# Performance work log

Measured on AMD Instinct MI355X. Metric: run time of the kernel, lower is better.

## Reference

```python
import jax, jax.numpy as jnp
import numpy as np

DIM = 512
NUM_HEADS = 8
WS = 7
HEAD_DIM = DIM // NUM_HEADS
SCALE = HEAD_DIM ** -0.5
THETA = 10000.0


def _freqs_cis_2d(hd, end):
    # 2D axial RoPE: interleaved (x,y) complex rotations per frequency
    Hg = int(end ** 0.5)
    pos = jnp.arange(end)
    x_pos = (pos % Hg).astype(jnp.float32)
    y_pos = (pos // Hg).astype(jnp.float32)
    freqs = 1.0 / THETA ** (jnp.arange(0, hd, 4)[: hd // 4].astype(jnp.float32) / hd)
    x_cis = jnp.exp(1j * jnp.outer(x_pos, freqs))  # (end, hd//4) complex64
    y_cis = jnp.exp(1j * jnp.outer(y_pos, freqs))
    return jnp.stack([x_cis, y_cis], axis=-1).reshape(end, -1)  # (end, hd//2)


def setup_inputs() -> dict:
    key = jax.random.key(0)
    k1, k2, k3 = jax.random.split(key, 3)
    B, H, W, C = 32, 56, 56, DIM
    x = jax.random.normal(k1, (B, H * W, C), dtype=jnp.float32)
    w_qkv = jax.random.normal(k2, (3 * C, C), dtype=jnp.float32) * 0.02
    w_proj = jax.random.normal(k3, (C, C), dtype=jnp.float32) * 0.02
    b_proj = jnp.zeros((C,), dtype=jnp.float32)
    return {"x": x, "w_qkv": w_qkv, "w_proj": w_proj, "b_proj": b_proj, "H": H, "W": W}


def reference(x, w_qkv, w_proj, b_proj, H, W):
    B, N, C = x.shape
    nh, hd, ws = NUM_HEADS, HEAD_DIM, WS
    _h, _w = H // ws, W // ws
    G, S = _h * _w, ws * ws
    # window partition: (B, _h, _w, ws, ws, C)
    xw = x.reshape(B, _h, ws, _w, ws, C).transpose(0, 1, 3, 2, 4, 5)
    qkv = jnp.einsum('bhwpqc,dc->bhwpqd', xw, w_qkv).reshape(B, G, S, 3, nh, hd)
    q, k, v = qkv[..., 0, :, :], qkv[..., 1, :, :], qkv[..., 2, :, :]  # (B,G,S,nh,hd)

    fc = _freqs_cis_2d(hd, S)  # (S, hd//2) complex64

    def rope(t):
        tc = t.reshape(*t.shape[:-1], hd // 2, 2)
        tc = jax.lax.complex(tc[..., 0], tc[..., 1])       # (B,G,S,nh,hd//2)
        tc = tc * fc[None, None, :, None, :]
        return jnp.stack([tc.real, tc.imag], axis=-1).reshape(t.shape)

    q = rope(q)
    k = rope(k)
    attn = jnp.einsum('bgsnd,bgtnd->bgnst', q, k) * SCALE  # (B,G,nh,S,S)
    attn = jax.nn.softmax(attn, axis=-1)
    out = jnp.einsum('bgnst,bgtnd->bgsnd', attn, v)        # (B,G,S,nh,hd)
    # window merge back to (B, H, W, C)
    out = out.reshape(B, _h, _w, ws, ws, C).transpose(0, 1, 3, 2, 4, 5).reshape(B, N, C)
    return jnp.einsum('bnc,dc->bnd', out, w_proj) + b_proj
```

## Files before the change

### kernel.cpp

```cpp
#include <hip/hip_runtime.h>
#include <stdint.h>
#include <stddef.h>

typedef _Float16 f16;
typedef _Float16 f16x8 __attribute__((ext_vector_type(8)));
typedef _Float16 f16x4 __attribute__((ext_vector_type(4)));
typedef float    f32x4 __attribute__((ext_vector_type(4)));

#define AS1 __attribute__((address_space(1)))
#define AS3 __attribute__((address_space(3)))

__device__ __forceinline__ void gl_lds16(const f16* g, f16* l) {
  __builtin_amdgcn_global_load_lds((const AS1 uint32_t*)g, (AS3 uint32_t*)l, 16, 0, 0);
}


__global__ __launch_bounds__(256) void k_prep(
    const float* __restrict__ x, const float* __restrict__ wqkv,
    const float* __restrict__ wproj,
    f16* __restrict__ x16, f16* __restrict__ wqkv16, f16* __restrict__ wproj16,
    float2* __restrict__ tab)
{
  const int XB = 25088, WQ = 384, WP = 128;
  int b = blockIdx.x, t = threadIdx.x;
  const float* src; f16* dst; long i0;
  if (b < XB)            { src = x;     dst = x16;     i0 = ((long)b*256 + t)*8; }
  else if (b < XB+WQ)    { src = wqkv;  dst = wqkv16;  i0 = ((long)(b-XB)*256 + t)*8; }
  else if (b < XB+WQ+WP) { src = wproj; dst = wproj16; i0 = ((long)(b-XB-WQ)*256 + t)*8; }
  else {
    int id = (b - XB - WQ - WP)*256 + t;
    if (id < 49*32) {
      int s = id >> 5, i = id & 31, j = i >> 1;
      float freq = expf(-(float)(4*j)*(1.0f/64.0f)*9.210340372f);
      float pos = (i & 1) ? (float)(s/7) : (float)(s%7);
      float a = pos * freq;
      tab[id] = make_float2(cosf(a), sinf(a));
    }
    return;
  }
  const float4* s4 = (const float4*)(src + i0);
  float4 v0 = s4[0], v1 = s4[1];
  f16x8 h = { (f16)v0.x,(f16)v0.y,(f16)v0.z,(f16)v0.w,
              (f16)v1.x,(f16)v1.y,(f16)v1.z,(f16)v1.w };
  *(f16x8*)(dst + i0) = h;
}

#define GEMM_STAGE(gW, gX, Wt, Xt, kt)                                        \
  {                                                                           \
    int srow = ln >> 3;                        \
    int schunk = (ln & 7) ^ srow;              \
    size_t goff = (size_t)srow * 512 + (kt)*64 + schunk * 8;                  \
    _Pragma("unroll")                                                         \
    for (int ii = 0; ii < 4; ++ii) {                                          \
      int r0 = wave * 32 + ii * 8;                                            \
      gl_lds16(gW + (size_t)r0 * 512 + goff, Wt + r0 * 64);                   \
      gl_lds16(gX + (size_t)r0 * 512 + goff, Xt + r0 * 64);                   \
    }                                                                         \
  }

#define GEMM_MAIN(Wt, Xt)                                                     \
  _Pragma("unroll")                                                           \
  for (int k2 = 0; k2 < 2; ++k2) {                                            \
    f16x8 af[4], bf[4];                                                       \
    int pc = ((k2 * 4 + quad) ^ (l15 & 7)) * 8;                               \
    _Pragma("unroll")                                                         \
    for (int i = 0; i < 4; ++i)                                               \
      af[i] = *(const f16x8*)&Wt[(wq * 64 + i * 16 + l15) * 64 + pc];         \
    _Pragma("unroll")                                                         \
    for (int j = 0; j < 4; ++j)                                               \
      bf[j] = *(const f16x8*)&Xt[(wp * 64 + j * 16 + l15) * 64 + pc];         \
    _Pragma("unroll")                                                         \
    for (int i = 0; i < 4; ++i)                                               \
      _Pragma("unroll")                                                       \
      for (int j = 0; j < 4; ++j)                                             \
        acc[i][j] = __builtin_amdgcn_mfma_f32_16x16x32_f16(af[i], bf[j],      \
                                                           acc[i][j], 0, 0, 0);\
  }

__global__ __launch_bounds__(256) void k_qkv(
    const f16* __restrict__ x16, const f16* __restrict__ w16,
    const float2* __restrict__ tab,
    f16* __restrict__ qb, f16* __restrict__ kb, f16* __restrict__ vb)
{
  __shared__ __align__(16) f16 Wt[128*64];
  __shared__ __align__(16) f16 Xt[128*64];
  const int by = blockIdx.x;
  const int bx = blockIdx.y;
  const int tid = threadIdx.x;
  const int wave = tid >> 6, ln = tid & 63;
  const int l15 = ln & 15, quad = ln >> 4;
  const int wq = wave >> 1, wp = wave & 1;

  f32x4 acc[4][4] = {};
  const f16* gW = w16 + (size_t)(by*128)*512;
  const f16* gX = x16 + (size_t)(bx*128)*512;

  for (int kt = 0; kt < 8; ++kt) {
    __syncthreads();
    GEMM_STAGE(gW, gX, Wt, Xt, kt);
    __syncthreads();
    GEMM_MAIN(Wt, Xt);
  }

  const int t = (by*128) >> 9;
#pragma unroll
  for (int j = 0; j < 4; ++j) {
    int m  = bx*128 + wp*64 + j*16 + l15;
    int b  = m / 3136;
    int nn = m - b*3136;
    int hh = nn / 56, ww = nn - hh*56;
    int gh = hh / 7,  p  = hh - gh*7;
    int gw = ww / 7,  qx = ww - gw*7;
    int g  = gh*8 + gw;
    int s  = p*7 + qx;
    int bg = b*64 + g;
#pragma unroll
    for (int i = 0; i < 4; ++i) {
      int c0   = by*128 + wq*64 + i*16 + quad*4;
      int cin  = c0 & 511;
      int head = cin >> 6;
      int dd   = cin & 63;
      float v0 = acc[i][j][0], v1 = acc[i][j][1], v2 = acc[i][j][2], v3 = acc[i][j][3];
      f16x4 h4;
      if (t < 2) {
        float2 t0 = tab[s*32 + (dd >> 1)];
        float2 t1 = tab[s*32 + (dd >> 1) + 1];
        h4[0] = (f16)(v0*t0.x - v1*t0.y);
        h4[1] = (f16)(v0*t0.y + v1*t0.x);
        h4[2] = (f16)(v2*t1.x - v3*t1.y);
        h4[3] = (f16)(v2*t1.y + v3*t1.x);
      } else {
        h4[0] = (f16)v0; h4[1] = (f16)v1; h4[2] = (f16)v2; h4[3] = (f16)v3;
      }
      f16* dst = (t == 0 ? qb : (t == 1 ? kb : vb))
               + (size_t)((bg*8 + head)*49 + s)*64 + dd;
      *(f16x4*)dst = h4;
    }
  }
}

__global__ __launch_bounds__(64) void k_attn(
    const f16* __restrict__ qb, const f16* __restrict__ kb,
    const f16* __restrict__ vb, f16* __restrict__ ob)
{
  __shared__ __align__(16) f16 Vt[64*64];
  __shared__ __align__(16) f16 P[64*72];
  __shared__ float lsum[64];
  const int bid = blockIdx.x;
  const int ln = threadIdx.x, l15 = ln & 15, quad = ln >> 4;
  const f16* q = qb + (size_t)bid*(49*64);
  const f16* k = kb + (size_t)bid*(49*64);
  const f16* v = vb + (size_t)bid*(49*64);

#pragma unroll
  for (int i = 0; i < 8; ++i)
    gl_lds16(v + (size_t)(i*8 + (ln>>3))*64 + (ln&7)*8, Vt + i*512);

  f32x4 a[4][4] = {};
#pragma unroll
  for (int kt = 0; kt < 2; ++kt) {
    f16x8 qf[4], kf[4];
#pragma unroll
    for (int mt = 0; mt < 4; ++mt) {
      int s = mt*16 + l15; if (s > 48) s = 48;
      qf[mt] = *(const f16x8*)(q + s*64 + kt*32 + quad*8);
      kf[mt] = *(const f16x8*)(k + s*64 + kt*32 + quad*8);
    }
#pragma unroll
    for (int mt = 0; mt < 4; ++mt)
#pragma unroll
      for (int nt = 0; nt < 4; ++nt)
        a[mt][nt] = __builtin_amdgcn_mfma_f32_16x16x32_f16(qf[mt], kf[nt], a[mt][nt], 0, 0, 0);
  }

  const float scale = 0.125f;
#pragma unroll
  for (int mt = 0; mt < 4; ++mt) {
    float mx[4] = {-1e30f,-1e30f,-1e30f,-1e30f};
#pragma unroll
    for (int nt = 0; nt < 4; ++nt) {
      int col = nt*16 + l15;
      bool valid = col < 49;
#pragma unroll
      for (int r = 0; r < 4; ++r) {
        float vv = valid ? a[mt][nt][r]*scale : -1e30f;
        a[mt][nt][r] = vv;
        mx[r] = fmaxf(mx[r], vv);
      }
    }
#pragma unroll
    for (int d = 1; d < 16; d <<= 1)
#pragma unroll
      for (int r = 0; r < 4; ++r) mx[r] = fmaxf(mx[r], __shfl_xor(mx[r], d, 64));
    float sm[4] = {0.f,0.f,0.f,0.f};
#pragma unroll
    for (int nt = 0; nt < 4; ++nt)
#pragma unroll
      for (int r = 0; r < 4; ++r) {
        float e = __expf(a[mt][nt][r] - mx[r]);
        a[mt][nt][r] = e;
        sm[r] += e;
      }
#pragma unroll
    for (int d = 1; d < 16; d <<= 1)
#pragma unroll
      for (int r = 0; r < 4; ++r) sm[r] += __shfl_xor(sm[r], d, 64);
#pragma unroll
    for (int nt = 0; nt < 4; ++nt)
#pragma unroll
      for (int r = 0; r < 4; ++r)
        P[(mt*16 + quad*4 + r)*72 + nt*16 + l15] = (f16)a[mt][nt][r];
    if (l15 == 0) {
#pragma unroll
      for (int r = 0; r < 4; ++r) lsum[mt*16 + quad*4 + r] = sm[r];
    }
  }
  __syncthreads();

  f32x4 o[4][4] = {};
#pragma unroll
  for (int kt = 0; kt < 2; ++kt) {
    const int s0 = kt*32 + quad*8;
    f16x8 vf[4], pf[4];
#pragma unroll
    for (int dt = 0; dt < 4; ++dt)
#pragma unroll
      for (int j = 0; j < 8; ++j)
        vf[dt][j] = Vt[(s0 + j)*64 + dt*16 + l15];
#pragma unroll
    for (int st = 0; st < 4; ++st) pf[st] = *(const f16x8*)&P[(st*16 + l15)*72 + s0];
#pragma unroll
    for (int dt = 0; dt < 4; ++dt)
#pragma unroll
      for (int st = 0; st < 4; ++st)
        o[dt][st] = __builtin_amdgcn_mfma_f32_16x16x32_f16(vf[dt], pf[st], o[dt][st], 0, 0, 0);
  }

  const int bg = bid >> 3, head = bid & 7;
#pragma unroll
  for (int st = 0; st < 4; ++st) {
    int sq = st*16 + l15;
    if (sq < 49) {
      float inv = 1.0f / lsum[sq];
#pragma unroll
      for (int dt = 0; dt < 4; ++dt) {
        int d0 = dt*16 + quad*4;
        f16x4 h4 = { (f16)(o[dt][st][0]*inv), (f16)(o[dt][st][1]*inv),
                     (f16)(o[dt][st][2]*inv), (f16)(o[dt][st][3]*inv) };
        *(f16x4*)(ob + (size_t)(bg*49 + sq)*512 + head*64 + d0) = h4;
      }
    }
  }
}

__global__ __launch_bounds__(256) void k_proj(
    const f16* __restrict__ a16, const f16* __restrict__ w16,
    const float* __restrict__ bias, float* __restrict__ out)
{
  __shared__ __align__(16) f16 Wt[128*64];
  __shared__ __align__(16) f16 Xt[128*64];
  const int by = blockIdx.x;
  const int bx = blockIdx.y;
  const int tid = threadIdx.x;
  const int wave = tid >> 6, ln = tid & 63;
  const int l15 = ln & 15, quad = ln >> 4;
  const int wq = wave >> 1, wp = wave & 1;

  f32x4 acc[4][4] = {};
  const f16* gW = w16 + (size_t)(by*128)*512;
  const f16* gX = a16 + (size_t)(bx*128)*512;

  for (int kt = 0; kt < 8; ++kt) {
    __syncthreads();
    GEMM_STAGE(gW, gX, Wt, Xt, kt);
    __syncthreads();
    GEMM_MAIN(Wt, Xt);
  }

#pragma unroll
  for (int j = 0; j < 4; ++j) {
    int m  = bx*128 + wp*64 + j*16 + l15;
    int b  = m / 3136;
    int rr = m - b*3136;
    int g  = rr / 49;
    int s  = rr - g*49;
    int gh = g >> 3, gw = g & 7;
    int p  = s / 7,  qx = s - p*7;
    int hh = gh*7 + p, ww = gw*7 + qx;
    size_t tok = (size_t)b*3136 + hh*56 + ww;
#pragma unroll
    for (int i = 0; i < 4; ++i) {
      int d0 = by*128 + wq*64 + i*16 + quad*4;
      float4 bb = *(const float4*)(bias + d0);
      float4 o4 = make_float4(acc[i][j][0]+bb.x, acc[i][j][1]+bb.y,
                              acc[i][j][2]+bb.z, acc[i][j][3]+bb.w);
      *(float4*)(out + tok*512 + d0) = o4;
    }
  }
}

extern "C" void kernel_launch(void* const* d_in, const int* in_sizes, int n_in,
                              void* d_out, int out_size, void* d_ws, size_t ws_size,
                              hipStream_t stream) {
  const float* x     = (const float*)d_in[0];
  const float* wqkv  = (const float*)d_in[1];
  const float* wproj = (const float*)d_in[2];
  const float* bias  = (const float*)d_in[3];

  char* ws = (char*)d_ws;
  f16*    x16   = (f16*)(ws);
  f16*    wq16  = (f16*)(ws + 102760448);
  f16*    wp16  = (f16*)(ws + 104333312);
  float2* tab   = (float2*)(ws + 104857600);
  f16*    vbuf  = (f16*)(ws + 104873984);
  f16*    attn16 = (f16*)(ws);

  f16* qbuf = (f16*)d_out;
  f16* kbuf = (f16*)((char*)d_out + 102760448);
  float* out = (float*)d_out;

  k_prep<<<dim3(25088 + 384 + 128 + 7), dim3(256), 0, stream>>>(
      x, wqkv, wproj, x16, wq16, wp16, tab);
  k_qkv<<<dim3(12, 784), dim3(256), 0, stream>>>(x16, wq16, tab, qbuf, kbuf, vbuf);
  k_attn<<<dim3(16384), dim3(64), 0, stream>>>(qbuf, kbuf, vbuf, attn16);
  k_proj<<<dim3(4, 784), dim3(256), 0, stream>>>(attn16, wp16, bias, out);
}
```

Before: 882.4 us.

## Double-buffer GEMM LDS tiles and remap block IDs for XCD-local reuse

The QKV and projection GEMMs now use two LDS buffers, prefetching the next K-tile with global_load_lds while MFMAs run on the current one. This removes one barrier per iteration and lets load latency overlap with compute. The grids become 1D, and block IDs are remapped so that blocks sharing the same X row tile land on the same XCD, which should improve L2 reuse. LDS use doubles to 64KB per block, which may lower occupancy, and per-lane global pointers are precomputed.

```diff
diff --git a/kernel.cpp b/kernel.cpp
--- a/kernel.cpp
+++ b/kernel.cpp
@@ -45,30 +45,37 @@
   *(f16x8*)(dst + i0) = h;
 }
 
-#define GEMM_STAGE(gW, gX, Wt, Xt, kt)                                        \
-  {                                                                           \
-    int srow = ln >> 3;                        \
-    int schunk = (ln & 7) ^ srow;              \
-    size_t goff = (size_t)srow * 512 + (kt)*64 + schunk * 8;                  \
-    _Pragma("unroll")                                                         \
-    for (int ii = 0; ii < 4; ++ii) {                                          \
-      int r0 = wave * 32 + ii * 8;                                            \
-      gl_lds16(gW + (size_t)r0 * 512 + goff, Wt + r0 * 64);                   \
-      gl_lds16(gX + (size_t)r0 * 512 + goff, Xt + r0 * 64);                   \
-    }                                                                         \
-  }
-
-#define GEMM_MAIN(Wt, Xt)                                                     \
+#define GEMM_PRELUDE()                                                        \
+  const int tid = threadIdx.x;                                                \
+  const int wave = tid >> 6, ln = tid & 63;                                   \
+  const int l15 = ln & 15, quad = ln >> 4;                                    \
+  const int wq = wave >> 1, wp = wave & 1;                                    \
+  const int srow = ln >> 3, schunk = (ln & 7) ^ srow;                         \
+  const f16* pW[4]; const f16* pX[4];                                         \
+  _Pragma("unroll")                                                           \
+  for (int ii = 0; ii < 4; ++ii) {                                            \
+    size_t ro = (size_t)(wave*32 + ii*8 + srow)*512 + schunk*8;               \
+    pW[ii] = gW + ro; pX[ii] = gX + ro;                                       \
+  }
+
+#define GEMM_STAGE(bsel, kt)                                                  \
+  _Pragma("unroll")                                                           \
+  for (int ii = 0; ii < 4; ++ii) {                                            \
+    gl_lds16(pW[ii] + (kt)*64, &Wt[bsel][(wave*32 + ii*8)*64]);               \
+    gl_lds16(pX[ii] + (kt)*64, &Xt[bsel][(wave*32 + ii*8)*64]);               \
+  }
+
+#define GEMM_MAIN(bsel)                                                       \
   _Pragma("unroll")                                                           \
   for (int k2 = 0; k2 < 2; ++k2) {                                            \
     f16x8 af[4], bf[4];                                                       \
     int pc = ((k2 * 4 + quad) ^ (l15 & 7)) * 8;                               \
     _Pragma("unroll")                                                         \
     for (int i = 0; i < 4; ++i)                                               \
-      af[i] = *(const f16x8*)&Wt[(wq * 64 + i * 16 + l15) * 64 + pc];         \
+      af[i] = *(const f16x8*)&Wt[bsel][(wq * 64 + i * 16 + l15) * 64 + pc];   \
     _Pragma("unroll")                                                         \
     for (int j = 0; j < 4; ++j)                                               \
-      bf[j] = *(const f16x8*)&Xt[(wp * 64 + j * 16 + l15) * 64 + pc];         \
+      bf[j] = *(const f16x8*)&Xt[bsel][(wp * 64 + j * 16 + l15) * 64 + pc];   \
     _Pragma("unroll")                                                         \
     for (int i = 0; i < 4; ++i)                                               \
       _Pragma("unroll")                                                       \
@@ -77,30 +84,36 @@
                                                            acc[i][j], 0, 0, 0);\
   }
 
+#define GEMM_LOOP()                                                           \
+  GEMM_STAGE(0, 0);                                                           \
+  __syncthreads();                                                            \
+  _Pragma("unroll")                                                           \
+  for (int kt = 0; kt < 8; ++kt) {                                            \
+    if (kt < 7) GEMM_STAGE((kt + 1) & 1, kt + 1);                             \
+    GEMM_MAIN(kt & 1);                                                        \
+    if (kt < 7) __syncthreads();                                              \
+  }
+
 __global__ __launch_bounds__(256) void k_qkv(
     const f16* __restrict__ x16, const f16* __restrict__ w16,
     const float2* __restrict__ tab,
     f16* __restrict__ qb, f16* __restrict__ kb, f16* __restrict__ vb)
 {
-  __shared__ __align__(16) f16 Wt[128*64];
-  __shared__ __align__(16) f16 Xt[128*64];
-  const int by = blockIdx.x;
-  const int bx = blockIdx.y;
-  const int tid = threadIdx.x;
-  const int wave = tid >> 6, ln = tid & 63;
-  const int l15 = ln & 15, quad = ln >> 4;
-  const int wq = wave >> 1, wp = wave & 1;
-
-  f32x4 acc[4][4] = {};
+  __shared__ __align__(16) f16 Wt[2][128*64];
+  __shared__ __align__(16) f16 Xt[2][128*64];
+  const int bid = blockIdx.x;
+  const int xcd = bid & 7;
+  const int jj  = bid >> 3;
+  const int qq  = jj / 12;
+  const int by  = jj - qq*12;
+  const int bx  = xcd + qq*8;
+
   const f16* gW = w16 + (size_t)(by*128)*512;
   const f16* gX = x16 + (size_t)(bx*128)*512;
-
-  for (int kt = 0; kt < 8; ++kt) {
-    __syncthreads();
-    GEMM_STAGE(gW, gX, Wt, Xt, kt);
-    __syncthreads();
-    GEMM_MAIN(Wt, Xt);
-  }
+  GEMM_PRELUDE();
+
+  f32x4 acc[4][4] = {};
+  GEMM_LOOP();
 
   const int t = (by*128) >> 9;
 #pragma unroll
@@ -257,25 +270,21 @@
     const f16* __restrict__ a16, const f16* __restrict__ w16,
     const float* __restrict__ bias, float* __restrict__ out)
 {
-  __shared__ __align__(16) f16 Wt[128*64];
-  __shared__ __align__(16) f16 Xt[128*64];
-  const int by = blockIdx.x;
-  const int bx = blockIdx.y;
-  const int tid = threadIdx.x;
-  const int wave = tid >> 6, ln = tid & 63;
-  const int l15 = ln & 15, quad = ln >> 4;
-  const int wq = wave >> 1, wp = wave & 1;
-
-  f32x4 acc[4][4] = {};
+  __shared__ __align__(16) f16 Wt[2][128*64];
+  __shared__ __align__(16) f16 Xt[2][128*64];
+  const int bid = blockIdx.x;
+  const int xcd = bid & 7;
+  const int jj  = bid >> 3;
+  const int qq  = jj >> 2;
+  const int by  = jj & 3;
+  const int bx  = xcd + qq*8;
+
   const f16* gW = w16 + (size_t)(by*128)*512;
   const f16* gX = a16 + (size_t)(bx*128)*512;
-
-  for (int kt = 0; kt < 8; ++kt) {
-    __syncthreads();
-    GEMM_STAGE(gW, gX, Wt, Xt, kt);
-    __syncthreads();
-    GEMM_MAIN(Wt, Xt);
-  }
+  GEMM_PRELUDE();
+
+  f32x4 acc[4][4] = {};
+  GEMM_LOOP();
 
 #pragma unroll
   for (int j = 0; j < 4; ++j) {
@@ -321,7 +330,7 @@
 
   k_prep<<<dim3(25088 + 384 + 128 + 7), dim3(256), 0, stream>>>(
       x, wqkv, wproj, x16, wq16, wp16, tab);
-  k_qkv<<<dim3(12, 784), dim3(256), 0, stream>>>(x16, wq16, tab, qbuf, kbuf, vbuf);
+  k_qkv<<<dim3(9408), dim3(256), 0, stream>>>(x16, wq16, tab, qbuf, kbuf, vbuf);
   k_attn<<<dim3(16384), dim3(64), 0, stream>>>(qbuf, kbuf, vbuf, attn16);
-  k_proj<<<dim3(4, 784), dim3(256), 0, stream>>>(attn16, wp16, bias, out);
-}
+  k_proj<<<dim3(3136), dim3(256), 0, stream>>>(attn16, wp16, bias, out);
+}
```

Measured after the change: 926.6 us. 5.0% more time.
